# Kernel tuning notes

Measured on AMD Instinct MI355X. Metric: run time of the kernel, lower is better.

## Reference

```python
import jax, jax.numpy as jnp
import numpy as np

THRESHOLD = 1.25
CURRENT_DECAY = 0.25
VOLTAGE_DECAY = 0.03
B, C_IN, C_HID, C_OUT, T = 16, 64 * 64 * 2, 512, 100, 300


def weight_norm(v, g):
    # per-output-neuron weight normalization: w = g * v / ||v||
    return g[:, None] * v / jnp.linalg.norm(v, axis=1, keepdims=True)


def spike_fn(volt):
    return (volt >= THRESHOLD).astype(volt.dtype)


def lif(z, cd, vd):
    # z: [B, C, T]  CUBA leaky integrate-and-fire recurrence over time
    zT = jnp.moveaxis(z, -1, 0)  # [T, B, C]
    zero = jnp.zeros_like(zT[0])

    def step(carry, zt):
        cur, volt = carry
        cur = (1.0 - cd) * cur + zt
        volt = (1.0 - vd) * volt + cur
        s = spike_fn(volt)
        volt = volt * (1.0 - s)  # reset on spike
        return (cur, volt), s

    _, sT = jax.lax.scan(step, (zero, zero), zT)
    return jnp.moveaxis(sT, 0, -1)  # [B, C, T]


def setup_inputs() -> dict:
    key = jax.random.key(0)
    ks = jax.random.split(key, 8)
    spike = (jax.random.uniform(ks[0], (B, C_IN, T)) < 0.02).astype(jnp.float32)
    s = 0.05
    return {
        "spike": spike,
        "v1": jax.random.normal(ks[1], (C_HID, C_IN), jnp.float32) * s,
        "g1": jnp.ones((C_HID,), jnp.float32),
        "v2": jax.random.normal(ks[2], (C_HID, C_HID), jnp.float32) * s,
        "g2": jnp.ones((C_HID,), jnp.float32),
        "v3": jax.random.normal(ks[3], (C_OUT, C_HID), jnp.float32) * s,
        "g3": jnp.ones((C_OUT,), jnp.float32),
        "current_decays": jnp.full((3,), CURRENT_DECAY, jnp.float32),
        "voltage_decays": jnp.full((3,), VOLTAGE_DECAY, jnp.float32),
    }


def reference(spike, v1, g1, v2, g2, v3, g3, current_decays, voltage_decays):
    x = spike
    for i, (v, g) in enumerate(((v1, g1), (v2, g2), (v3, g3))):
        w = weight_norm(v, g)                      # [out, in]
        z = jnp.einsum("oi,bit->bot", w, x)        # synapse
        x = lif(z, current_decays[i], voltage_decays[i])  # CUBA neuron
    return x
```

## Files before the change

### kernel.cpp

```cpp
#include <hip/hip_runtime.h>
#include <stdint.h>
#include <math.h>

#define NB   16
#define CIN  8192
#define CHID 512
#define COUT 100
#define TT   300
#define TG4  4
#define NTG4 75
#define NW1  256
#define EVCAP1 384
#define EVCAP2 512

__global__ void norm_kernel(const float* __restrict__ v, float* __restrict__ nrm, int cin) {
    int row = blockIdx.x;
    const float* vr = v + (size_t)row * cin;
    float s = 0.f;
    for (int i = threadIdx.x; i < cin; i += 256) {
        float x = vr[i];
        s = __fadd_rn(s, __fmul_rn(x, x));
    }
    __shared__ float red[256];
    red[threadIdx.x] = s;
    __syncthreads();
    for (int off = 128; off > 0; off >>= 1) {
        if (threadIdx.x < off) red[threadIdx.x] += red[threadIdx.x + off];
        __syncthreads();
    }
    if (threadIdx.x == 0) nrm[row] = sqrtf(red[0]);
}

template<int WS>
__global__ void trans_kernel(const float* __restrict__ v, const float* __restrict__ g,
                             const float* __restrict__ nrm, float* __restrict__ wt,
                             int RO, int CI) {
    __shared__ float tile[32][33];
    int i0 = blockIdx.x * 32, o0 = blockIdx.y * 32;
    int tx = threadIdx.x, ty = threadIdx.y;
    for (int k = 0; k < 32; k += 8) {
        int o = o0 + ty + k, i = i0 + tx;
        float val = 0.f;
        if (o < RO) val = __fmul_rn(v[(size_t)o * CI + i], g[o]) / nrm[o];
        tile[ty + k][tx] = val;
    }
    __syncthreads();
    for (int k = 0; k < 32; k += 8) {
        int i = i0 + ty + k, oo = o0 + tx;
        if (oo < WS) wt[(size_t)i * WS + oo] = tile[tx][ty + k];
    }
}

__global__ __launch_bounds__(256) void mask_kernel(const float* __restrict__ spike,
                                                   uint32_t* __restrict__ maskT) {
    __shared__ uint32_t flag[64][16];
    int b = blockIdx.x, itile = blockIdx.y;
    int tid = threadIdx.x;
    int row = tid >> 2, qc = tid & 3;
    const float* sp = spike + ((size_t)(b * CIN + itile * 64 + row)) * TT;
    for (int tc = 0; tc < 5; ++tc) {
        #pragma unroll
        for (int k = 0; k < 4; ++k) {
            int t0 = tc * 64 + k * 16 + qc * 4;
            uint32_t packed = 0;
            if (t0 + 3 < TT) {
                float4 v = *(const float4*)(sp + t0);
                packed = (v.x != 0.f ? 1u : 0u) | (v.y != 0.f ? 0x100u : 0u)
                       | (v.z != 0.f ? 0x10000u : 0u) | (v.w != 0.f ? 0x1000000u : 0u);
            }
            flag[row][k * 4 + qc] = packed;
        }
        __syncthreads();
        if (tid < 128) {
            int t_l = tid >> 1, half = tid & 1;
            int t = tc * 64 + t_l;
            if (t < TT) {
                uint32_t word = 0;
                #pragma unroll
                for (int k = 0; k < 32; ++k) {
                    uint32_t f = flag[half * 32 + k][t_l >> 2];
                    word |= (((f >> ((t_l & 3) * 8)) & 1u) << k);
                }
                maskT[((size_t)b * TT + t) * NW1 + itile * 2 + half] = word;
            }
        }
        __syncthreads();
    }
}

__global__ __launch_bounds__(256) void evmerge1_kernel(const uint32_t* __restrict__ maskT,
                                                       uint32_t* __restrict__ ev,
                                                       int* __restrict__ cnt) {
    int b = blockIdx.x, tg = blockIdx.y;
    int tid = threadIdx.x, lane = tid & 63, wv = tid >> 6;
    int t = tg * TG4 + wv;
    size_t bt = (size_t)b * TT + t;
    const uint32_t* mrow = maskT + bt * NW1;
    uint4 w4 = *(const uint4*)(mrow + lane * 4);
    int c = __popc(w4.x) + __popc(w4.y) + __popc(w4.z) + __popc(w4.w);
    int off = c;
    for (int d = 1; d < 64; d <<= 1) {
        int nn = __shfl_up(off, d, 64);
        if (lane >= d) off += nn;
    }
    int total = __shfl(off, 63, 64);
    off -= c;
    uint32_t* erow = ev + bt * EVCAP1;
    uint32_t wsv[4] = {w4.x, w4.y, w4.z, w4.w};
    int base_i = lane * 128;
    #pragma unroll
    for (int wi = 0; wi < 4; ++wi) {
        uint32_t m = wsv[wi];
        while (m) {
            int bpos = __builtin_ctz(m);
            m &= m - 1;
            if (off < EVCAP1) erow[off] = (uint32_t)(base_i + wi * 32 + bpos) << 11;
            ++off;
        }
    }
    if (lane == 63) cnt[bt] = (total < EVCAP1 ? total : EVCAP1);
}

template<int WS, int EVCAP>
__global__ __launch_bounds__(256) void zg_kernel(const uint32_t* __restrict__ ev,
                                                 const int* __restrict__ cnt,
                                                 const float* __restrict__ wt,
                                                 float* __restrict__ zout) {
    int oslice = blockIdx.x, b = blockIdx.y, tg = blockIdx.z;
    int tid = threadIdx.x, lane = tid & 63, wv = tid >> 6;
    int t = tg * TG4 + wv;
    size_t bt = (size_t)b * TT + t;
    const uint32_t* erow = ev + bt * EVCAP;
    int n = cnt[bt];
    const char* wb = (const char*)wt + (size_t)oslice * 256;
    uint32_t lane4 = (uint32_t)lane * 4u;
    float acc = 0.f;
    int j = 0;
    for (; j + 16 <= n; j += 16) {
        uint4 eA = *(const uint4*)(erow + j);
        uint4 eB = *(const uint4*)(erow + j + 4);
        uint4 eC = *(const uint4*)(erow + j + 8);
        uint4 eD = *(const uint4*)(erow + j + 12);
        float w0  = *(const float*)(wb + (size_t)(eA.x + lane4));
        float w1  = *(const float*)(wb + (size_t)(eA.y + lane4));
        float w2  = *(const float*)(wb + (size_t)(eA.z + lane4));
        float w3  = *(const float*)(wb + (size_t)(eA.w + lane4));
        float w4  = *(const float*)(wb + (size_t)(eB.x + lane4));
        float w5  = *(const float*)(wb + (size_t)(eB.y + lane4));
        float w6  = *(const float*)(wb + (size_t)(eB.z + lane4));
        float w7  = *(const float*)(wb + (size_t)(eB.w + lane4));
        float w8  = *(const float*)(wb + (size_t)(eC.x + lane4));
        float w9  = *(const float*)(wb + (size_t)(eC.y + lane4));
        float w10 = *(const float*)(wb + (size_t)(eC.z + lane4));
        float w11 = *(const float*)(wb + (size_t)(eC.w + lane4));
        float w12 = *(const float*)(wb + (size_t)(eD.x + lane4));
        float w13 = *(const float*)(wb + (size_t)(eD.y + lane4));
        float w14 = *(const float*)(wb + (size_t)(eD.z + lane4));
        float w15 = *(const float*)(wb + (size_t)(eD.w + lane4));
        acc += w0;  acc += w1;  acc += w2;  acc += w3;
        acc += w4;  acc += w5;  acc += w6;  acc += w7;
        acc += w8;  acc += w9;  acc += w10; acc += w11;
        acc += w12; acc += w13; acc += w14; acc += w15;
    }
    for (; j + 4 <= n; j += 4) {
        uint4 e = *(const uint4*)(erow + j);
        float w0 = *(const float*)(wb + (size_t)(e.x + lane4));
        float w1 = *(const float*)(wb + (size_t)(e.y + lane4));
        float w2 = *(const float*)(wb + (size_t)(e.z + lane4));
        float w3 = *(const float*)(wb + (size_t)(e.w + lane4));
        acc += w0; acc += w1; acc += w2; acc += w3;
    }
    for (; j < n; ++j)
        acc += *(const float*)(wb + (size_t)(erow[j] + lane4));
    __builtin_nontemporal_store(acc, zout + bt * WS + oslice * 64 + lane);
}

__global__ __launch_bounds__(64) void lif_ev_kernel(const float* __restrict__ z,
                                                    uint64_t* __restrict__ msk,
                                                    const float* __restrict__ cdarr,
                                                    const float* __restrict__ vdarr,
                                                    int li) {
    int bid = blockIdx.x;
    int b = bid >> 3, oseg = bid & 7;
    int lane = threadIdx.x;
    int o = oseg * 64 + lane;
    float omc = 1.0f - cdarr[li];
    float omv = 1.0f - vdarr[li];
    float cur = 0.f, volt = 0.f;
    const float* zp = z + (size_t)b * TT * CHID + o;

    float A[10], Bv[10];
    auto loadg = [&](float (&buf)[10], int g) {
        #pragma unroll
        for (int k = 0; k < 10; ++k) buf[k] = zp[(size_t)(g * 10 + k) * CHID];
    };
    auto stepg = [&](float (&buf)[10], int g) {
        #pragma unroll
        for (int k = 0; k < 10; ++k) {
            int t = g * 10 + k;
            cur  = __fadd_rn(__fmul_rn(omc, cur), buf[k]);
            volt = __fadd_rn(__fmul_rn(omv, volt), cur);
            bool s = (volt >= 1.25f);
            volt = s ? 0.f : volt;
            uint64_t bal = __ballot(s);
            if (lane == 0) msk[((size_t)b * TT + t) * 8 + oseg] = bal;
        }
    };
    loadg(A, 0);
    for (int g = 0; g < 30; g += 2) {
        if (g + 1 < 30) loadg(Bv, g + 1);
        stepg(A, g);
        if (g + 2 < 30) loadg(A, g + 2);
        if (g + 1 < 30) stepg(Bv, g + 1);
    }
}

__global__ __launch_bounds__(256) void evbuild2_kernel(const uint64_t* __restrict__ msk,
                                                       uint32_t* __restrict__ ev,
                                                       int* __restrict__ cnt, int shift) {
    int b = blockIdx.x, tg = blockIdx.y;
    int tid = threadIdx.x, lane = tid & 63, wv = tid >> 6;
    int t = tg * TG4 + wv;
    size_t bt = (size_t)b * TT + t;
    uint64_t word = msk[bt * 8 + (lane >> 3)];
    uint32_t byte = (uint32_t)(word >> ((lane & 7) * 8)) & 0xFFu;
    int c = __popc(byte);
    int off = c;
    for (int d = 1; d < 64; d <<= 1) {
        int nn = __shfl_up(off, d, 64);
        if (lane >= d) off += nn;
    }
    int total = __shfl(off, 63, 64);
    off -= c;
    uint32_t* erow = ev + bt * EVCAP2;
    int obase = lane * 8;
    while (byte) {
        int k = __builtin_ctz(byte);
        byte &= byte - 1;
        erow[off++] = (uint32_t)(obase + k) << shift;
    }
    if (lane == 63) cnt[bt] = total;
}

__global__ __launch_bounds__(64) void lif_out_kernel(const float* __restrict__ z,
                                                     float* __restrict__ out,
                                                     const float* __restrict__ cdarr,
                                                     const float* __restrict__ vdarr,
                                                     int li) {
    int gid = blockIdx.x * 64 + threadIdx.x;
    if (gid >= NB * COUT) return;
    int b = gid / COUT, o = gid % COUT;
    float omc = 1.0f - cdarr[li];
    float omv = 1.0f - vdarr[li];
    float cur = 0.f, volt = 0.f;
    const float* zp = z + (size_t)b * TT * 128 + o;
    float* op = out + ((size_t)b * COUT + o) * TT;

    float A[10], Bv[10];
    auto loadg = [&](float (&buf)[10], int g) {
        #pragma unroll
        for (int k = 0; k < 10; ++k) buf[k] = zp[(size_t)(g * 10 + k) * 128];
    };
    auto stepg = [&](float (&buf)[10], int g) {
        #pragma unroll
        for (int k = 0; k < 10; ++k) {
            cur  = __fadd_rn(__fmul_rn(omc, cur), buf[k]);
            volt = __fadd_rn(__fmul_rn(omv, volt), cur);
            bool s = (volt >= 1.25f);
            volt = s ? 0.f : volt;
            op[g * 10 + k] = s ? 1.0f : 0.0f;
        }
    };
    loadg(A, 0);
    for (int g = 0; g < 30; g += 2) {
        if (g + 1 < 30) loadg(Bv, g + 1);
        stepg(A, g);
        if (g + 2 < 30) loadg(A, g + 2);
        if (g + 1 < 30) stepg(Bv, g + 1);
    }
}

extern "C" void kernel_launch(void* const* d_in, const int* in_sizes, int n_in,
                              void* d_out, int out_size, void* d_ws, size_t ws_size,
                              hipStream_t stream) {
    const float* spike = (const float*)d_in[0];
    const float* v1 = (const float*)d_in[1];
    const float* g1 = (const float*)d_in[2];
    const float* v2 = (const float*)d_in[3];
    const float* g2 = (const float*)d_in[4];
    const float* v3 = (const float*)d_in[5];
    const float* g3 = (const float*)d_in[6];
    const float* cd = (const float*)d_in[7];
    const float* vd = (const float*)d_in[8];

    float* ws   = (float*)d_ws;
    float* w1t  = ws;
    float* w2t  = w1t + (size_t)CIN * CHID;
    float* w3t  = w2t + (size_t)CHID * CHID;
    float* nrm1 = w3t + (size_t)CHID * 128;
    float* nrm2 = nrm1 + 512;
    float* nrm3 = nrm2 + 512;
    float* zbuf = nrm3 + 128;
    float* z3   = zbuf + (size_t)NB * TT * CHID;
    uint32_t* evb   = (uint32_t*)(z3 + (size_t)NB * TT * 128);
    int*      cntb  = (int*)(evb + (size_t)NB * TT * EVCAP2);
    uint64_t* mskb  = (uint64_t*)(cntb + (size_t)NB * TT);
    uint32_t* maskT = (uint32_t*)(mskb + (size_t)NB * TT * 8);
    size_t need = (size_t)((uint8_t*)(maskT + (size_t)NB * TT * NW1) - (uint8_t*)d_ws);
    if (ws_size < need) return;

    norm_kernel<<<dim3(CHID), dim3(256), 0, stream>>>(v1, nrm1, CIN);
    norm_kernel<<<dim3(CHID), dim3(256), 0, stream>>>(v2, nrm2, CHID);
    norm_kernel<<<dim3(COUT), dim3(256), 0, stream>>>(v3, nrm3, CHID);
    trans_kernel<512><<<dim3(CIN / 32, CHID / 32), dim3(32, 8), 0, stream>>>(v1, g1, nrm1, w1t, CHID, CIN);
    trans_kernel<512><<<dim3(CHID / 32, CHID / 32), dim3(32, 8), 0, stream>>>(v2, g2, nrm2, w2t, CHID, CHID);
    trans_kernel<128><<<dim3(CHID / 32, 4), dim3(32, 8), 0, stream>>>(v3, g3, nrm3, w3t, COUT, CHID);

    mask_kernel<<<dim3(NB, CIN / 64), dim3(256), 0, stream>>>(spike, maskT);
    evmerge1_kernel<<<dim3(NB, NTG4), dim3(256), 0, stream>>>(maskT, evb, cntb);
    zg_kernel<512, EVCAP1><<<dim3(8, NB, NTG4), dim3(256), 0, stream>>>(evb, cntb, w1t, zbuf);
    lif_ev_kernel<<<dim3(NB * 8), dim3(64), 0, stream>>>(zbuf, mskb, cd, vd, 0);
    evbuild2_kernel<<<dim3(NB, NTG4), dim3(256), 0, stream>>>(mskb, evb, cntb, 11);
    zg_kernel<512, EVCAP2><<<dim3(8, NB, NTG4), dim3(256), 0, stream>>>(evb, cntb, w2t, zbuf);
    lif_ev_kernel<<<dim3(NB * 8), dim3(64), 0, stream>>>(zbuf, mskb, cd, vd, 1);
    evbuild2_kernel<<<dim3(NB, NTG4), dim3(256), 0, stream>>>(mskb, evb, cntb, 9);
    zg_kernel<128, EVCAP2><<<dim3(2, NB, NTG4), dim3(256), 0, stream>>>(evb, cntb, w3t, z3);
    lif_out_kernel<<<dim3((NB * COUT + 63) / 64), dim3(64), 0, stream>>>(z3, (float*)d_out, cd, vd, 2);
}
```

Before: 251.6 us.

## Merge norm kernels, deepen gather unroll, nontemporal spike loads

Folds the three per-layer norm launches into one kernel that picks its matrix by block index, saving two launches. The spike loads in the mask kernel become nontemporal, since that data is streamed once. The sparse-weight gather loop now unrolls to 32 events per iteration to keep more loads in flight, and the z output store goes back to a normal cached store so the following LIF kernel can hit in L2. The wider unroll raises register pressure and may reduce occupancy.

```diff
diff --git a/kernel.cpp b/kernel.cpp
--- a/kernel.cpp
+++ b/kernel.cpp
@@ -13,8 +13,19 @@
 #define EVCAP1 384
 #define EVCAP2 512
 
-__global__ void norm_kernel(const float* __restrict__ v, float* __restrict__ nrm, int cin) {
-    int row = blockIdx.x;
+typedef float fx4 __attribute__((ext_vector_type(4)));
+
+__global__ __launch_bounds__(256) void norm3_kernel(const float* __restrict__ v1,
+                                                    const float* __restrict__ v2,
+                                                    const float* __restrict__ v3,
+                                                    float* __restrict__ nrm1,
+                                                    float* __restrict__ nrm2,
+                                                    float* __restrict__ nrm3) {
+    int blk = blockIdx.x;
+    const float* v; float* out; int cin, row;
+    if (blk < 512)       { v = v1; out = nrm1; cin = CIN;  row = blk; }
+    else if (blk < 1024) { v = v2; out = nrm2; cin = CHID; row = blk - 512; }
+    else                 { v = v3; out = nrm3; cin = CHID; row = blk - 1024; }
     const float* vr = v + (size_t)row * cin;
     float s = 0.f;
     for (int i = threadIdx.x; i < cin; i += 256) {
@@ -28,7 +39,7 @@
         if (threadIdx.x < off) red[threadIdx.x] += red[threadIdx.x + off];
         __syncthreads();
     }
-    if (threadIdx.x == 0) nrm[row] = sqrtf(red[0]);
+    if (threadIdx.x == 0) out[row] = sqrtf(red[0]);
 }
 
 template<int WS>
@@ -64,7 +75,7 @@
             int t0 = tc * 64 + k * 16 + qc * 4;
             uint32_t packed = 0;
             if (t0 + 3 < TT) {
-                float4 v = *(const float4*)(sp + t0);
+                fx4 v = __builtin_nontemporal_load((const fx4*)(sp + t0));
                 packed = (v.x != 0.f ? 1u : 0u) | (v.y != 0.f ? 0x100u : 0u)
                        | (v.z != 0.f ? 0x10000u : 0u) | (v.w != 0.f ? 0x1000000u : 0u);
             }
@@ -136,43 +147,38 @@
     uint32_t lane4 = (uint32_t)lane * 4u;
     float acc = 0.f;
     int j = 0;
-    for (; j + 16 <= n; j += 16) {
+    for (; j + 32 <= n; j += 32) {
+        uint4 e[8];
+        #pragma unroll
+        for (int q = 0; q < 8; ++q) e[q] = *(const uint4*)(erow + j + 4 * q);
+        float w[32];
+        #pragma unroll
+        for (int q = 0; q < 8; ++q) {
+            w[4 * q + 0] = *(const float*)(wb + (size_t)(e[q].x + lane4));
+            w[4 * q + 1] = *(const float*)(wb + (size_t)(e[q].y + lane4));
+            w[4 * q + 2] = *(const float*)(wb + (size_t)(e[q].z + lane4));
+            w[4 * q + 3] = *(const float*)(wb + (size_t)(e[q].w + lane4));
+        }
+        #pragma unroll
+        for (int q = 0; q < 32; ++q) acc += w[q];
+    }
+    for (; j + 8 <= n; j += 8) {
         uint4 eA = *(const uint4*)(erow + j);
         uint4 eB = *(const uint4*)(erow + j + 4);
-        uint4 eC = *(const uint4*)(erow + j + 8);
-        uint4 eD = *(const uint4*)(erow + j + 12);
-        float w0  = *(const float*)(wb + (size_t)(eA.x + lane4));
-        float w1  = *(const float*)(wb + (size_t)(eA.y + lane4));
-        float w2  = *(const float*)(wb + (size_t)(eA.z + lane4));
-        float w3  = *(const float*)(wb + (size_t)(eA.w + lane4));
-        float w4  = *(const float*)(wb + (size_t)(eB.x + lane4));
-        float w5  = *(const float*)(wb + (size_t)(eB.y + lane4));
-        float w6  = *(const float*)(wb + (size_t)(eB.z + lane4));
-        float w7  = *(const float*)(wb + (size_t)(eB.w + lane4));
-        float w8  = *(const float*)(wb + (size_t)(eC.x + lane4));
-        float w9  = *(const float*)(wb + (size_t)(eC.y + lane4));
-        float w10 = *(const float*)(wb + (size_t)(eC.z + lane4));
-        float w11 = *(const float*)(wb + (size_t)(eC.w + lane4));
-        float w12 = *(const float*)(wb + (size_t)(eD.x + lane4));
-        float w13 = *(const float*)(wb + (size_t)(eD.y + lane4));
-        float w14 = *(const float*)(wb + (size_t)(eD.z + lane4));
-        float w15 = *(const float*)(wb + (size_t)(eD.w + lane4));
-        acc += w0;  acc += w1;  acc += w2;  acc += w3;
-        acc += w4;  acc += w5;  acc += w6;  acc += w7;
-        acc += w8;  acc += w9;  acc += w10; acc += w11;
-        acc += w12; acc += w13; acc += w14; acc += w15;
-    }
-    for (; j + 4 <= n; j += 4) {
-        uint4 e = *(const uint4*)(erow + j);
-        float w0 = *(const float*)(wb + (size_t)(e.x + lane4));
-        float w1 = *(const float*)(wb + (size_t)(e.y + lane4));
-        float w2 = *(const float*)(wb + (size_t)(e.z + lane4));
-        float w3 = *(const float*)(wb + (size_t)(e.w + lane4));
+        float w0 = *(const float*)(wb + (size_t)(eA.x + lane4));
+        float w1 = *(const float*)(wb + (size_t)(eA.y + lane4));
+        float w2 = *(const float*)(wb + (size_t)(eA.z + lane4));
+        float w3 = *(const float*)(wb + (size_t)(eA.w + lane4));
+        float w4 = *(const float*)(wb + (size_t)(eB.x + lane4));
+        float w5 = *(const float*)(wb + (size_t)(eB.y + lane4));
+        float w6 = *(const float*)(wb + (size_t)(eB.z + lane4));
+        float w7 = *(const float*)(wb + (size_t)(eB.w + lane4));
         acc += w0; acc += w1; acc += w2; acc += w3;
+        acc += w4; acc += w5; acc += w6; acc += w7;
     }
     for (; j < n; ++j)
         acc += *(const float*)(wb + (size_t)(erow[j] + lane4));
-    __builtin_nontemporal_store(acc, zout + bt * WS + oslice * 64 + lane);
+    zout[bt * WS + oslice * 64 + lane] = acc;
 }
 
 __global__ __launch_bounds__(64) void lif_ev_kernel(const float* __restrict__ z,
@@ -309,9 +315,7 @@
     size_t need = (size_t)((uint8_t*)(maskT + (size_t)NB * TT * NW1) - (uint8_t*)d_ws);
     if (ws_size < need) return;
 
-    norm_kernel<<<dim3(CHID), dim3(256), 0, stream>>>(v1, nrm1, CIN);
-    norm_kernel<<<dim3(CHID), dim3(256), 0, stream>>>(v2, nrm2, CHID);
-    norm_kernel<<<dim3(COUT), dim3(256), 0, stream>>>(v3, nrm3, CHID);
+    norm3_kernel<<<dim3(512 + 512 + 100), dim3(256), 0, stream>>>(v1, v2, v3, nrm1, nrm2, nrm3);
     trans_kernel<512><<<dim3(CIN / 32, CHID / 32), dim3(32, 8), 0, stream>>>(v1, g1, nrm1, w1t, CHID, CIN);
     trans_kernel<512><<<dim3(CHID / 32, CHID / 32), dim3(32, 8), 0, stream>>>(v2, g2, nrm2, w2t, CHID, CHID);
     trans_kernel<128><<<dim3(CHID / 32, 4), dim3(32, 8), 0, stream>>>(v3, g3, nrm3, w3t, COUT, CHID);
```

New measurement: 257.2 us. 1.02x slower.
